# Performance work log

Measured on AMD Instinct MI355X. Metric: run time of the kernel, lower is better.

## Reference

```python
import jax, jax.numpy as jnp
import numpy as np

BETA = 0.25


def setup_inputs() -> dict:
    key = jax.random.key(0)
    k1, k2 = jax.random.split(key)
    z = jax.random.normal(k1, (16, 2048, 256), dtype=jnp.float32)
    # n_q=4 codebooks, each [n_e=2048, e_dim=256]; xavier-ish scale
    W = jax.random.normal(k2, (4, 2048, 256), dtype=jnp.float32) * 0.05
    return {"z": z, "W": W}


def reference(z, W):
    """Residual VQ forward (p=1.0, eval-mode math). Returns (z_q, loss, indices)."""
    n_q, n_e, e_dim = W.shape
    lead = z.shape[:-1]
    flat_shape = (-1, e_dim)

    residual = z
    cumulative_q = jnp.zeros_like(z)
    losses = []
    idx_list = []
    for k in range(n_q):
        Wk = W[k]  # [n_e, e_dim]
        flat = residual.reshape(flat_shape)  # [N, e_dim]
        dist = (
            jnp.sum(flat * flat, axis=1, keepdims=True)
            - 2.0 * (flat @ Wk.T)
            + jnp.sum(Wk * Wk, axis=1)[None, :]
        )
        idx = jnp.argmin(dist, axis=1)  # [N]
        # one_hot @ Wk is mathematically a gather of codebook rows
        q = Wk[idx].reshape(residual.shape)
        # commit + beta*codebook; both are (residual.detach() - q)^2.mean(-1)
        diff = jax.lax.stop_gradient(residual) - q
        losses.append((1.0 + BETA) * jnp.mean(diff * diff, axis=-1))
        cumulative_q = cumulative_q + q
        residual = residual - q
        idx_list.append(idx.reshape(*lead, 1))

    # straight-through: gradient of z_q flows only to z
    z_q = z + jax.lax.stop_gradient(cumulative_q - z)
    total_loss = jnp.mean(jnp.stack(losses, axis=0).mean(axis=0))
    indices = jnp.concatenate(idx_list, axis=-1)  # [..., n_q]
    return z_q, total_loss, indices
```

## Files before the change

kernel.cpp:

```cpp
#include <hip/hip_runtime.h>
#include <cstdint>
#include <math.h>
#include <float.h>

#define N_Q   4
#define NROWS 32768
#define EDIM  256
#define NE    2048
#define NCT_H 64
#define TM    64
#define NTHREADS 256

#define ZQ_SIZE  (NROWS * EDIM)
#define LOSS_OFF ZQ_SIZE
#define IDX_OFF  (ZQ_SIZE + 1)

#define TAU 0.012f

typedef __attribute__((ext_vector_type(8))) _Float16 f16x8;
typedef __attribute__((ext_vector_type(4))) float    f32x4;

union F8 { _Float16 h[8]; f16x8 v; };

__device__ __forceinline__ float np_block128_sq(const float* __restrict__ p) {
    #pragma clang fp contract(off)
    float r[8];
    #pragma unroll
    for (int j = 0; j < 8; ++j) { float v = p[j]; r[j] = v * v; }
    for (int i = 8; i < 128; i += 8) {
        #pragma unroll
        for (int j = 0; j < 8; ++j) { float v = p[i + j]; float sq = v * v; r[j] = r[j] + sq; }
    }
    return ((r[0] + r[1]) + (r[2] + r[3])) + ((r[4] + r[5]) + (r[6] + r[7]));
}

__global__ __launch_bounds__(256) void wsq_kernel(const float* __restrict__ W,
                                                  float* __restrict__ wsq32) {
    __shared__ float rowbuf[4][EDIM];
    int wv   = threadIdx.x >> 6;
    int row  = blockIdx.x * 4 + (threadIdx.x >> 6);
    int lane = threadIdx.x & 63;
    float4 v = ((const float4*)(W + (size_t)row * EDIM))[lane];
    *(float4*)&rowbuf[wv][lane * 4] = v;
    __syncthreads();
    if (lane == 0) {
        float a = np_block128_sq(rowbuf[wv]);
        float b = np_block128_sq(rowbuf[wv] + 128);
        wsq32[row] = a + b;
    }
}

__global__ __launch_bounds__(256) void wh_kernel(const float* __restrict__ W,
                                                 short* __restrict__ wh) {
    int gid  = blockIdx.x * 256 + threadIdx.x;
    int lane = gid & 63;
    int grp  = gid >> 6;
    int ctq  = grp >> 3;
    int ks   = grp & 7;
    int n = lane & 15, kq = lane >> 4;
    const float* src = W + (((size_t)(ctq * 16 + n)) << 8) + ks * 32 + kq * 8;
    float4 p0 = *(const float4*)src;
    float4 p1 = *(const float4*)(src + 4);
    float v[8] = {p0.x, p0.y, p0.z, p0.w, p1.x, p1.y, p1.z, p1.w};
    F8 h;
    #pragma unroll
    for (int j = 0; j < 8; ++j) h.h[j] = (_Float16)v[j];
    *(f16x8*)(wh + (((size_t)grp) << 9) + lane * 8) = h.v;
}

__device__ __forceinline__ void top3_merge(float& a1, int& ai1, float& a2, int& ai2, float& a3,
                                           float b1, int bi1, float b2, int bi2, float b3) {
    float c1, c2, c3; int k1, k2;
    if (b1 < a1 || (b1 == a1 && bi1 < ai1)) {
        c1 = b1; k1 = bi1;
        if (a1 < b2 || (a1 == b2 && ai1 < bi2)) { c2 = a1; k2 = ai1; c3 = fminf(b2, a2); }
        else                                    { c2 = b2; k2 = bi2; c3 = fminf(a1, b3); }
    } else {
        c1 = a1; k1 = ai1;
        if (b1 < a2 || (b1 == a2 && bi1 < ai2)) { c2 = b1; k2 = bi1; c3 = fminf(a2, b2); }
        else                                    { c2 = a2; k2 = ai2; c3 = fminf(b1, a3); }
    }
    a1 = c1; ai1 = k1; a2 = c2; ai2 = k2; a3 = c3;
}

__global__ __launch_bounds__(256, 2) void rvq_main(
    const float* __restrict__ z, const float* __restrict__ W,
    const float* __restrict__ wsq32, const short* __restrict__ wh,
    float* __restrict__ resd_g, float* __restrict__ out,
    float* __restrict__ loss_partial)
{
    __shared__ __align__(16) short lds_b[2][2][4][512];
    __shared__ float Srow[TM];
    __shared__ float rm1[2][TM], rm2[2][TM], rm3[2][TM];
    __shared__ int   ri1[2][TM], ri2[2][TM];
    __shared__ int   idx_s[TM], is2_s[TM];
    __shared__ int   rk_cnt, rk_list[TM];
    __shared__ int   pr_cnt, pr_list[TM];
    __shared__ float rrow_s[EDIM];
    __shared__ float red_f[NTHREADS];
    __shared__ int   red_i[NTHREADS];
    __shared__ float wavesum[4];

    const int tid  = threadIdx.x;
    const int wave = tid >> 6;
    const int lane = tid & 63;
    const int n    = lane & 15;
    const int kq   = lane >> 4;
    const int half = wave >> 1;
    const int rsel = wave & 1;
    const int row0 = blockIdx.x * TM;
    const int rowg = row0 + rsel * 32;

    for (int i = tid; i < TM * 64; i += NTHREADS) {
        int r = i >> 6, c = i & 63;
        ((float4*)resd_g)[(((size_t)(row0 + r)) << 6) + c] =
            ((const float4*)z)[(((size_t)(row0 + r)) << 6) + c];
    }

    float lsum = 0.f;

    for (int q = 0; q < N_Q; ++q) {
        const float* Wk   = W + (size_t)q * NE * EDIM;
        const float* wsqk = wsq32 + q * NE;
        const short* whq  = wh + ((size_t)q << 19);

        __syncthreads();
        if (tid == 0) { rk_cnt = 0; pr_cnt = 0; }
        if (tid < 2 * TM) {
            int r = tid >> 1, hf = tid & 1;
            float s = np_block128_sq(resd_g + (((size_t)(row0 + r)) << 8) + hf * 128);
            float s2 = __shfl_xor(s, 1, 64);
            if (hf == 0) Srow[r] = s + s2;
        }
        __syncthreads();

        f16x8 ah[2][8], al[2][8];
        #pragma unroll
        for (int t = 0; t < 2; ++t) {
            #pragma unroll
            for (int ks = 0; ks < 8; ++ks) {
                const float* rp = resd_g + (((size_t)(rowg + t * 16 + n)) << 8) + ks * 32 + kq * 8;
                float4 p0 = *(const float4*)rp;
                float4 p1 = *(const float4*)(rp + 4);
                float v[8] = {p0.x, p0.y, p0.z, p0.w, p1.x, p1.y, p1.z, p1.w};
                F8 h, l;
                #pragma unroll
                for (int j = 0; j < 8; ++j) {
                    _Float16 hb = (_Float16)v[j];
                    h.h[j] = hb;
                    l.h[j] = (_Float16)(v[j] - (float)hb);
                }
                ah[t][ks] = h.v; al[t][ks] = l.v;
            }
        }
        float sreg[2][4];
        #pragma unroll
        for (int t = 0; t < 2; ++t)
            #pragma unroll
            for (int rg = 0; rg < 4; ++rg)
                sreg[t][rg] = Srow[rsel * 32 + t * 16 + kq * 4 + rg];

        float M1[8], M2[8], M3[8]; int I1[8], I2[8];
        #pragma unroll
        for (int s = 0; s < 8; ++s) {
            M1[s] = INFINITY; M2[s] = INFINITY; M3[s] = INFINITY; I1[s] = 0; I2[s] = 0;
        }

        auto stage = [&](int buf, int ct, int kp) {
            #pragma unroll
            for (int j = 0; j < 2; ++j) {
                int ksl = (wave & 1) * 2 + j;
                size_t grp = ((size_t)((wave >> 1) * 64 + ct) << 3) + kp * 4 + ksl;
                const short* gp = whq + (grp << 9) + lane * 8;
                __builtin_amdgcn_global_load_lds(
                    (const __attribute__((address_space(1))) void*)gp,
                    (__attribute__((address_space(3))) void*)&lds_b[buf][wave >> 1][ksl][0],
                    16, 0, 0);
            }
        };

        f32x4 acc[2][2];
        stage(0, 0, 0);
        __syncthreads();

        for (int ct = 0; ct < NCT_H; ++ct) {
            float wq = wsqk[(half * 64 + ct) * 16 + n];

            stage(1, ct, 1);
            #pragma unroll
            for (int t = 0; t < 2; ++t) {
                acc[t][0] = (f32x4){0.f, 0.f, 0.f, 0.f};
                acc[t][1] = (f32x4){0.f, 0.f, 0.f, 0.f};
            }
            #pragma unroll
            for (int ksl = 0; ksl < 4; ++ksl) {
                f16x8 bh = *(const f16x8*)&lds_b[0][half][ksl][lane * 8];
                const int c = ksl & 1;
                acc[0][c] = __builtin_amdgcn_mfma_f32_16x16x32_f16(ah[0][ksl], bh, acc[0][c], 0, 0, 0);
                acc[0][c] = __builtin_amdgcn_mfma_f32_16x16x32_f16(al[0][ksl], bh, acc[0][c], 0, 0, 0);
                acc[1][c] = __builtin_amdgcn_mfma_f32_16x16x32_f16(ah[1][ksl], bh, acc[1][c], 0, 0, 0);
                acc[1][c] = __builtin_amdgcn_mfma_f32_16x16x32_f16(al[1][ksl], bh, acc[1][c], 0, 0, 0);
            }
            __syncthreads();

            if (ct + 1 < NCT_H) stage(0, ct + 1, 0);
            #pragma unroll
            for (int ksl = 0; ksl < 4; ++ksl) {
                f16x8 bh = *(const f16x8*)&lds_b[1][half][ksl][lane * 8];
                const int ks = 4 + ksl, c = ksl & 1;
                acc[0][c] = __builtin_amdgcn_mfma_f32_16x16x32_f16(ah[0][ks], bh, acc[0][c], 0, 0, 0);
                acc[0][c] = __builtin_amdgcn_mfma_f32_16x16x32_f16(al[0][ks], bh, acc[0][c], 0, 0, 0);
                acc[1][c] = __builtin_amdgcn_mfma_f32_16x16x32_f16(ah[1][ks], bh, acc[1][c], 0, 0, 0);
                acc[1][c] = __builtin_amdgcn_mfma_f32_16x16x32_f16(al[1][ks], bh, acc[1][c], 0, 0, 0);
            }

            int cg = (half * 64 + ct) * 16 + n;
            #pragma unroll
            for (int t = 0; t < 2; ++t) {
                #pragma unroll
                for (int rg = 0; rg < 4; ++rg) {
                    float g = acc[t][0][rg] + acc[t][1][rg];
                    float d = fmaf(-2.0f, g, sreg[t][rg]) + wq;
                    int s = t * 4 + rg;
                    bool c1 = d < M1[s];
                    bool c2 = d < M2[s];
                    M3[s] = fminf(M3[s], fmaxf(M2[s], d));
                    M2[s] = fminf(M2[s], fmaxf(M1[s], d));
                    I2[s] = c1 ? I1[s] : (c2 ? cg : I2[s]);
                    M1[s] = fminf(M1[s], d);
                    I1[s] = c1 ? cg : I1[s];
                }
            }
            __syncthreads();
        }

        #pragma unroll
        for (int s = 0; s < 8; ++s) {
            float a1 = M1[s], a2 = M2[s], a3 = M3[s]; int ai = I1[s], aj = I2[s];
            #pragma unroll
            for (int mask = 1; mask < 16; mask <<= 1) {
                float b1 = __shfl_xor(a1, mask, 64);
                float b2 = __shfl_xor(a2, mask, 64);
                float b3 = __shfl_xor(a3, mask, 64);
                int   bi = __shfl_xor(ai, mask, 64);
                int   bj = __shfl_xor(aj, mask, 64);
                top3_merge(a1, ai, a2, aj, a3, b1, bi, b2, bj, b3);
            }
            if (n == 0) {
                int rr = rsel * 32 + (s >> 2) * 16 + kq * 4 + (s & 3);
                rm1[half][rr] = a1; rm2[half][rr] = a2; rm3[half][rr] = a3;
                ri1[half][rr] = ai; ri2[half][rr] = aj;
            }
        }
        __syncthreads();

        if (tid < TM) {
            float a1 = rm1[0][tid], a2 = rm2[0][tid], a3 = rm3[0][tid];
            int ai = ri1[0][tid], aj = ri2[0][tid];
            top3_merge(a1, ai, a2, aj, a3,
                       rm1[1][tid], ri1[1][tid], rm2[1][tid], ri2[1][tid], rm3[1][tid]);
            idx_s[tid] = ai; is2_s[tid] = aj;
            if (a2 - a1 <= TAU) {
                if (a3 - a1 > TAU) { int p = atomicAdd(&pr_cnt, 1); pr_list[p] = tid; }
                else               { int p = atomicAdd(&rk_cnt, 1); rk_list[p] = tid; }
            }
        }
        __syncthreads();

        {
            int ncheck = rk_cnt;
            for (int f = 0; f < ncheck; ++f) {
                int r = rk_list[f];
                if (tid < 64)
                    ((float4*)rrow_s)[tid] =
                        ((const float4*)(resd_g + (((size_t)(row0 + r)) << 8)))[tid];
                __syncthreads();
                float Sr = Srow[r];
                float accv[8];
                #pragma unroll
                for (int j = 0; j < 8; ++j) accv[j] = 0.f;
                const float* wp = Wk + ((size_t)tid * 8) * EDIM;
                for (int kb = 0; kb < 64; ++kb) {
                    float4 rv = *(const float4*)&rrow_s[kb * 4];
                    #pragma unroll
                    for (int j = 0; j < 8; ++j) {
                        float4 wv = *(const float4*)(wp + j * EDIM + kb * 4);
                        accv[j] = fmaf(rv.x, wv.x, accv[j]);
                        accv[j] = fmaf(rv.y, wv.y, accv[j]);
                        accv[j] = fmaf(rv.z, wv.z, accv[j]);
                        accv[j] = fmaf(rv.w, wv.w, accv[j]);
                    }
                }
                float bm = FLT_MAX; int bi = 0;
                #pragma unroll
                for (int j = 0; j < 8; ++j) {
                    int c = tid * 8 + j;
                    float d = fmaf(-2.0f, accv[j], Sr) + wsqk[c];
                    if (d < bm) { bm = d; bi = c; }
                }
                red_f[tid] = bm; red_i[tid] = bi;
                __syncthreads();
                for (int off = 128; off > 0; off >>= 1) {
                    if (tid < off) {
                        float v = red_f[tid + off]; int ii = red_i[tid + off];
                        if (v < red_f[tid] || (v == red_f[tid] && ii < red_i[tid])) {
                            red_f[tid] = v; red_i[tid] = ii;
                        }
                    }
                    __syncthreads();
                }
                if (tid == 0) idx_s[r] = red_i[0];
                __syncthreads();
            }
        }

        {
            int cnt2 = pr_cnt * 2;
            for (int base = 0; base < cnt2; base += NTHREADS) {
                int slot = base + tid;
                float d = FLT_MAX; int code = 0; int r = -1;
                if (slot < cnt2) {
                    r = pr_list[slot >> 1];
                    code = (slot & 1) ? is2_s[r] : idx_s[r];
                    const float* rp = resd_g + (((size_t)(row0 + r)) << 8);
                    const float* wp = Wk + ((size_t)code << 8);
                    float acc1 = 0.f;
                    for (int kb = 0; kb < 64; ++kb) {
                        float4 rv = *(const float4*)(rp + kb * 4);
                        float4 wv = *(const float4*)(wp + kb * 4);
                        acc1 = fmaf(rv.x, wv.x, acc1);
                        acc1 = fmaf(rv.y, wv.y, acc1);
                        acc1 = fmaf(rv.z, wv.z, acc1);
                        acc1 = fmaf(rv.w, wv.w, acc1);
                    }
                    d = fmaf(-2.0f, acc1, Srow[r]) + wsqk[code];
                }
                float dp = __shfl_xor(d, 1, 64);
                int   cp = __shfl_xor(code, 1, 64);
                if (slot < cnt2 && (slot & 1) == 0) {
                    idx_s[r] = (dp < d || (dp == d && cp < code)) ? cp : code;
                }
            }
        }
        __syncthreads();

        if (tid < TM)
            out[IDX_OFF + (size_t)(row0 + tid) * N_Q + q] = (float)idx_s[tid];
        __syncthreads();

        {
            const int d = tid;
            for (int r = 0; r < TM; ++r) {
                float w = Wk[(((size_t)idx_s[r]) << 8) + d];
                float* rp = resd_g + (((size_t)(row0 + r)) << 8) + d;
                float nv = *rp - w;
                *rp = nv;
                lsum = fmaf(nv, nv, lsum);
            }
        }
    }

    __syncthreads();
    for (int i = tid; i < TM * 64; i += NTHREADS) {
        int r = i >> 6, c = i & 63;
        float4 zv = ((const float4*)z)[(((size_t)(row0 + r)) << 6) + c];
        float4 rv = ((const float4*)resd_g)[(((size_t)(row0 + r)) << 6) + c];
        float4 o = {zv.x - rv.x, zv.y - rv.y, zv.z - rv.z, zv.w - rv.w};
        ((float4*)out)[(((size_t)(row0 + r)) << 6) + c] = o;
    }
    #pragma unroll
    for (int off = 32; off > 0; off >>= 1) lsum += __shfl_down(lsum, off, 64);
    if (lane == 0) wavesum[wave] = lsum;
    __syncthreads();
    if (tid == 0)
        loss_partial[blockIdx.x] = wavesum[0] + wavesum[1] + wavesum[2] + wavesum[3];
}

__global__ __launch_bounds__(256) void loss_reduce(const float* __restrict__ partial,
                                                   float* __restrict__ out) {
    __shared__ float sh[256];
    int t = threadIdx.x;
    sh[t] = partial[t] + partial[t + 256];
    __syncthreads();
    for (int off = 128; off > 0; off >>= 1) {
        if (t < off) sh[t] += sh[t + off];
        __syncthreads();
    }
    if (t == 0)
        out[LOSS_OFF] = sh[0] * (1.25f / ((float)N_Q * (float)NROWS * (float)EDIM));
}

extern "C" void kernel_launch(void* const* d_in, const int* in_sizes, int n_in,
                              void* d_out, int out_size, void* d_ws, size_t ws_size,
                              hipStream_t stream) {
    const float* z = (const float*)d_in[0];
    const float* W = (const float*)d_in[1];
    float* out = (float*)d_out;

    float* wsq32   = (float*)d_ws;
    float* partial = (float*)((char*)d_ws + 32768);
    short* wh      = (short*)((char*)d_ws + 65536);
    float* resd    = (float*)((char*)d_ws + 65536 + 8388608);

    hipLaunchKernelGGL(wsq_kernel, dim3(NE * N_Q / 4), dim3(NTHREADS), 0, stream, W, wsq32);
    hipLaunchKernelGGL(wh_kernel, dim3(1024), dim3(NTHREADS), 0, stream, W, wh);
    hipLaunchKernelGGL(rvq_main, dim3(NROWS / TM), dim3(NTHREADS), 0, stream,
                       z, W, wsq32, wh, resd, out, partial);
    hipLaunchKernelGGL(loss_reduce, dim3(1), dim3(NTHREADS), 0, stream, partial, out);
}
```

Before: 717.1 us.

## Deepen codebook staging to 4-buffer ring with one barrier per tile

Replaces the two half-tile double buffer, which needed two block barriers per column tile, with a four-slot LDS ring that prefetches two tiles ahead. Each iteration uses explicit vmcnt waits and a single barrier. Codebook squared norms are also preloaded into LDS, and MFMA sections are given raised wave priority. This grows LDS use, which may hurt occupancy at two blocks per CU, and the hand-written vmcnt counts must match the number of outstanding loads exactly.

```diff
diff --git a/kernel.cpp b/kernel.cpp
--- a/kernel.cpp
+++ b/kernel.cpp
@@ -89,7 +89,8 @@
     float* __restrict__ resd_g, float* __restrict__ out,
     float* __restrict__ loss_partial)
 {
-    __shared__ __align__(16) short lds_b[2][2][4][512];
+    __shared__ __align__(16) short lds_b[4][2][8][512];
+    __shared__ float wsq_lds[2 * 1024];
     __shared__ float Srow[TM];
     __shared__ float rm1[2][TM], rm2[2][TM], rm3[2][TM];
     __shared__ int   ri1[2][TM], ri2[2][TM];
@@ -132,7 +133,29 @@
             float s2 = __shfl_xor(s, 1, 64);
             if (hf == 0) Srow[r] = s + s2;
         }
-        __syncthreads();
+        for (int i = tid; i < 512; i += NTHREADS)
+            ((float4*)wsq_lds)[i] = ((const float4*)wsqk)[i];
+        __syncthreads();
+
+        auto stage = [&](int ctn) {
+            int b = ctn & 3;
+            #pragma unroll
+            for (int kp = 0; kp < 2; ++kp) {
+                #pragma unroll
+                for (int j = 0; j < 2; ++j) {
+                    int ksl = (wave & 1) * 2 + j;
+                    size_t grp = ((size_t)(half * 64 + ctn) << 3) + kp * 4 + ksl;
+                    const short* gp = whq + (grp << 9) + lane * 8;
+                    __builtin_amdgcn_global_load_lds(
+                        (const __attribute__((address_space(1))) void*)gp,
+                        (__attribute__((address_space(3))) void*)&lds_b[b][half][kp * 4 + ksl][0],
+                        16, 0, 0);
+                }
+            }
+        };
+
+        stage(0);
+        stage(1);
 
         f16x8 ah[2][8], al[2][8];
         #pragma unroll
@@ -166,54 +189,26 @@
             M1[s] = INFINITY; M2[s] = INFINITY; M3[s] = INFINITY; I1[s] = 0; I2[s] = 0;
         }
 
-        auto stage = [&](int buf, int ct, int kp) {
-            #pragma unroll
-            for (int j = 0; j < 2; ++j) {
-                int ksl = (wave & 1) * 2 + j;
-                size_t grp = ((size_t)((wave >> 1) * 64 + ct) << 3) + kp * 4 + ksl;
-                const short* gp = whq + (grp << 9) + lane * 8;
-                __builtin_amdgcn_global_load_lds(
-                    (const __attribute__((address_space(1))) void*)gp,
-                    (__attribute__((address_space(3))) void*)&lds_b[buf][wave >> 1][ksl][0],
-                    16, 0, 0);
-            }
-        };
-
-        f32x4 acc[2][2];
-        stage(0, 0, 0);
-        __syncthreads();
-
-        for (int ct = 0; ct < NCT_H; ++ct) {
-            float wq = wsqk[(half * 64 + ct) * 16 + n];
-
-            stage(1, ct, 1);
+        auto body = [&](int ct) {
+            float wq = wsq_lds[half * 1024 + ct * 16 + n];
+            const int b = ct & 3;
+            f32x4 acc[2][2];
             #pragma unroll
             for (int t = 0; t < 2; ++t) {
                 acc[t][0] = (f32x4){0.f, 0.f, 0.f, 0.f};
                 acc[t][1] = (f32x4){0.f, 0.f, 0.f, 0.f};
             }
-            #pragma unroll
-            for (int ksl = 0; ksl < 4; ++ksl) {
-                f16x8 bh = *(const f16x8*)&lds_b[0][half][ksl][lane * 8];
-                const int c = ksl & 1;
-                acc[0][c] = __builtin_amdgcn_mfma_f32_16x16x32_f16(ah[0][ksl], bh, acc[0][c], 0, 0, 0);
-                acc[0][c] = __builtin_amdgcn_mfma_f32_16x16x32_f16(al[0][ksl], bh, acc[0][c], 0, 0, 0);
-                acc[1][c] = __builtin_amdgcn_mfma_f32_16x16x32_f16(ah[1][ksl], bh, acc[1][c], 0, 0, 0);
-                acc[1][c] = __builtin_amdgcn_mfma_f32_16x16x32_f16(al[1][ksl], bh, acc[1][c], 0, 0, 0);
-            }
-            __syncthreads();
-
-            if (ct + 1 < NCT_H) stage(0, ct + 1, 0);
-            #pragma unroll
-            for (int ksl = 0; ksl < 4; ++ksl) {
-                f16x8 bh = *(const f16x8*)&lds_b[1][half][ksl][lane * 8];
-                const int ks = 4 + ksl, c = ksl & 1;
+            __builtin_amdgcn_s_setprio(1);
+            #pragma unroll
+            for (int ks = 0; ks < 8; ++ks) {
+                f16x8 bh = *(const f16x8*)&lds_b[b][half][ks][lane * 8];
+                const int c = ks & 1;
                 acc[0][c] = __builtin_amdgcn_mfma_f32_16x16x32_f16(ah[0][ks], bh, acc[0][c], 0, 0, 0);
                 acc[0][c] = __builtin_amdgcn_mfma_f32_16x16x32_f16(al[0][ks], bh, acc[0][c], 0, 0, 0);
                 acc[1][c] = __builtin_amdgcn_mfma_f32_16x16x32_f16(ah[1][ks], bh, acc[1][c], 0, 0, 0);
                 acc[1][c] = __builtin_amdgcn_mfma_f32_16x16x32_f16(al[1][ks], bh, acc[1][c], 0, 0, 0);
             }
-
+            __builtin_amdgcn_s_setprio(0);
             int cg = (half * 64 + ct) * 16 + n;
             #pragma unroll
             for (int t = 0; t < 2; ++t) {
@@ -231,7 +226,29 @@
                     I1[s] = c1 ? cg : I1[s];
                 }
             }
-            __syncthreads();
+        };
+
+        for (int ct = 0; ct < NCT_H - 2; ++ct) {
+            stage(ct + 2);
+            __builtin_amdgcn_sched_barrier(0);
+            asm volatile("s_waitcnt vmcnt(8)" ::: "memory");
+            __builtin_amdgcn_s_barrier();
+            __builtin_amdgcn_sched_barrier(0);
+            body(ct);
+        }
+        {
+            __builtin_amdgcn_sched_barrier(0);
+            asm volatile("s_waitcnt vmcnt(4)" ::: "memory");
+            __builtin_amdgcn_s_barrier();
+            __builtin_amdgcn_sched_barrier(0);
+            body(NCT_H - 2);
+        }
+        {
+            __builtin_amdgcn_sched_barrier(0);
+            asm volatile("s_waitcnt vmcnt(0)" ::: "memory");
+            __builtin_amdgcn_s_barrier();
+            __builtin_amdgcn_sched_barrier(0);
+            body(NCT_H - 1);
         }
 
         #pragma unroll
```

New measurement: 899.2 us. 25.4% more time.

## Drop fp16 low-residual split, stage two code tiles per phase with double buffering

Applied to the files above, without the earlier changes.

Removes the hi/lo fp16 split of the residual so each distance GEMM uses one fp16 MFMA per k-step instead of two, halving tensor-core work. It also restructures codebook staging to load two full-K code tiles per phase into a larger double-buffered LDS region, cutting barriers per tile. Codebook prefetch is issued before the residual conversion to overlap. Lower precision may change argmin choices, though the existing top-3 candidate / refine path (tau) likely catches near ties.

```diff
diff --git a/kernel.cpp b/kernel.cpp
--- a/kernel.cpp
+++ b/kernel.cpp
@@ -8,6 +8,7 @@
 #define EDIM  256
 #define NE    2048
 #define NCT_H 64
+#define NPH   32
 #define TM    64
 #define NTHREADS 256
 
@@ -89,7 +90,7 @@
     float* __restrict__ resd_g, float* __restrict__ out,
     float* __restrict__ loss_partial)
 {
-    __shared__ __align__(16) short lds_b[2][2][4][512];
+    __shared__ __align__(16) short lds_b[2][2][16][512];
     __shared__ float Srow[TM];
     __shared__ float rm1[2][TM], rm2[2][TM], rm3[2][TM];
     __shared__ int   ri1[2][TM], ri2[2][TM];
@@ -132,9 +133,26 @@
             float s2 = __shfl_xor(s, 1, 64);
             if (hf == 0) Srow[r] = s + s2;
         }
-        __syncthreads();
-
-        f16x8 ah[2][8], al[2][8];
+
+        auto stage = [&](int buf, int ct0) {
+            #pragma unroll
+            for (int ctp = 0; ctp < 2; ++ctp) {
+                #pragma unroll
+                for (int j = 0; j < 4; ++j) {
+                    int ks = (wave & 1) * 4 + j;
+                    size_t grp = ((size_t)(half * 64 + ct0 + ctp) << 3) + ks;
+                    const short* gp = whq + (grp << 9) + lane * 8;
+                    __builtin_amdgcn_global_load_lds(
+                        (const __attribute__((address_space(1))) void*)gp,
+                        (__attribute__((address_space(3))) void*)&lds_b[buf][half][ctp * 8 + ks][0],
+                        16, 0, 0);
+                }
+            }
+        };
+
+        stage(0, 0);
+
+        f16x8 ah[2][8];
         #pragma unroll
         for (int t = 0; t < 2; ++t) {
             #pragma unroll
@@ -143,16 +161,14 @@
                 float4 p0 = *(const float4*)rp;
                 float4 p1 = *(const float4*)(rp + 4);
                 float v[8] = {p0.x, p0.y, p0.z, p0.w, p1.x, p1.y, p1.z, p1.w};
-                F8 h, l;
-                #pragma unroll
-                for (int j = 0; j < 8; ++j) {
-                    _Float16 hb = (_Float16)v[j];
-                    h.h[j] = hb;
-                    l.h[j] = (_Float16)(v[j] - (float)hb);
-                }
-                ah[t][ks] = h.v; al[t][ks] = l.v;
-            }
-        }
+                F8 h;
+                #pragma unroll
+                for (int j = 0; j < 8; ++j) h.h[j] = (_Float16)v[j];
+                ah[t][ks] = h.v;
+            }
+        }
+        __syncthreads();
+
         float sreg[2][4];
         #pragma unroll
         for (int t = 0; t < 2; ++t)
@@ -166,71 +182,42 @@
             M1[s] = INFINITY; M2[s] = INFINITY; M3[s] = INFINITY; I1[s] = 0; I2[s] = 0;
         }
 
-        auto stage = [&](int buf, int ct, int kp) {
-            #pragma unroll
-            for (int j = 0; j < 2; ++j) {
-                int ksl = (wave & 1) * 2 + j;
-                size_t grp = ((size_t)((wave >> 1) * 64 + ct) << 3) + kp * 4 + ksl;
-                const short* gp = whq + (grp << 9) + lane * 8;
-                __builtin_amdgcn_global_load_lds(
-                    (const __attribute__((address_space(1))) void*)gp,
-                    (__attribute__((address_space(3))) void*)&lds_b[buf][wave >> 1][ksl][0],
-                    16, 0, 0);
+        auto body = [&](int buf, int ct0) {
+            #pragma unroll
+            for (int ctp = 0; ctp < 2; ++ctp) {
+                int ct = ct0 + ctp;
+                float wq = wsqk[(half * 64 + ct) * 16 + n];
+                f32x4 acc[2];
+                acc[0] = (f32x4){0.f, 0.f, 0.f, 0.f};
+                acc[1] = (f32x4){0.f, 0.f, 0.f, 0.f};
+                #pragma unroll
+                for (int ks = 0; ks < 8; ++ks) {
+                    f16x8 bh = *(const f16x8*)&lds_b[buf][half][ctp * 8 + ks][lane * 8];
+                    acc[0] = __builtin_amdgcn_mfma_f32_16x16x32_f16(ah[0][ks], bh, acc[0], 0, 0, 0);
+                    acc[1] = __builtin_amdgcn_mfma_f32_16x16x32_f16(ah[1][ks], bh, acc[1], 0, 0, 0);
+                }
+                int cg = (half * 64 + ct) * 16 + n;
+                #pragma unroll
+                for (int t = 0; t < 2; ++t) {
+                    #pragma unroll
+                    for (int rg = 0; rg < 4; ++rg) {
+                        float d = fmaf(-2.0f, acc[t][rg], sreg[t][rg]) + wq;
+                        int s = t * 4 + rg;
+                        bool c1 = d < M1[s];
+                        bool c2 = d < M2[s];
+                        M3[s] = fminf(M3[s], fmaxf(M2[s], d));
+                        M2[s] = fminf(M2[s], fmaxf(M1[s], d));
+                        I2[s] = c1 ? I1[s] : (c2 ? cg : I2[s]);
+                        M1[s] = fminf(M1[s], d);
+                        I1[s] = c1 ? cg : I1[s];
+                    }
+                }
             }
         };
 
-        f32x4 acc[2][2];
-        stage(0, 0, 0);
-        __syncthreads();
-
-        for (int ct = 0; ct < NCT_H; ++ct) {
-            float wq = wsqk[(half * 64 + ct) * 16 + n];
-
-            stage(1, ct, 1);
-            #pragma unroll
-            for (int t = 0; t < 2; ++t) {
-                acc[t][0] = (f32x4){0.f, 0.f, 0.f, 0.f};
-                acc[t][1] = (f32x4){0.f, 0.f, 0.f, 0.f};
-            }
-            #pragma unroll
-            for (int ksl = 0; ksl < 4; ++ksl) {
-                f16x8 bh = *(const f16x8*)&lds_b[0][half][ksl][lane * 8];
-                const int c = ksl & 1;
-                acc[0][c] = __builtin_amdgcn_mfma_f32_16x16x32_f16(ah[0][ksl], bh, acc[0][c], 0, 0, 0);
-                acc[0][c] = __builtin_amdgcn_mfma_f32_16x16x32_f16(al[0][ksl], bh, acc[0][c], 0, 0, 0);
-                acc[1][c] = __builtin_amdgcn_mfma_f32_16x16x32_f16(ah[1][ksl], bh, acc[1][c], 0, 0, 0);
-                acc[1][c] = __builtin_amdgcn_mfma_f32_16x16x32_f16(al[1][ksl], bh, acc[1][c], 0, 0, 0);
-            }
-            __syncthreads();
-
-            if (ct + 1 < NCT_H) stage(0, ct + 1, 0);
-            #pragma unroll
-            for (int ksl = 0; ksl < 4; ++ksl) {
-                f16x8 bh = *(const f16x8*)&lds_b[1][half][ksl][lane * 8];
-                const int ks = 4 + ksl, c = ksl & 1;
-                acc[0][c] = __builtin_amdgcn_mfma_f32_16x16x32_f16(ah[0][ks], bh, acc[0][c], 0, 0, 0);
-                acc[0][c] = __builtin_amdgcn_mfma_f32_16x16x32_f16(al[0][ks], bh, acc[0][c], 0, 0, 0);
-                acc[1][c] = __builtin_amdgcn_mfma_f32_16x16x32_f16(ah[1][ks], bh, acc[1][c], 0, 0, 0);
-                acc[1][c] = __builtin_amdgcn_mfma_f32_16x16x32_f16(al[1][ks], bh, acc[1][c], 0, 0, 0);
-            }
-
-            int cg = (half * 64 + ct) * 16 + n;
-            #pragma unroll
-            for (int t = 0; t < 2; ++t) {
-                #pragma unroll
-                for (int rg = 0; rg < 4; ++rg) {
-                    float g = acc[t][0][rg] + acc[t][1][rg];
-                    float d = fmaf(-2.0f, g, sreg[t][rg]) + wq;
-                    int s = t * 4 + rg;
-                    bool c1 = d < M1[s];
-                    bool c2 = d < M2[s];
-                    M3[s] = fminf(M3[s], fmaxf(M2[s], d));
-                    M2[s] = fminf(M2[s], fmaxf(M1[s], d));
-                    I2[s] = c1 ? I1[s] : (c2 ? cg : I2[s]);
-                    M1[s] = fminf(M1[s], d);
-                    I1[s] = c1 ? cg : I1[s];
-                }
-            }
+        for (int p = 0; p < NPH; ++p) {
+            if (p + 1 < NPH) stage((p + 1) & 1, (p + 1) * 2);
+            body(p & 1, p * 2);
             __syncthreads();
         }
 
```

After: 791.4 us. 10.4% more time.
